# Kernel tuning notes

Hardware: AMD Instinct MI355X
Metric: run time of the kernel (lower is better)

Reference implementation:

```python
import jax, jax.numpy as jnp
import numpy as np

# ---- static config (from init_kwargs) ----
N = 500_000            # total points
B = 4                  # batch size (lidar frames)
VX, VY, VZ = 0.2, 0.2, 4.0
PC = (0.0, -40.0, -3.0, 70.4, 40.0, 1.0)  # point cloud range
NZ = int((PC[5] - PC[2]) / VZ)   # 1
NY = int((PC[4] - PC[1]) / VY)   # 400
NX = int((PC[3] - PC[0]) / VX)   # 352
CANVAS = B * NZ * NY * NX        # dense voxel canvas (563200)
EPS = 1e-3                       # BN eps
XOFF = VX / 2 + PC[0]
YOFF = VY / 2 + PC[1]
ZOFF = VZ / 2 + PC[2]
C0, C1 = 64, 128                 # feat_channels
CIN = 13                         # 4 + 2(spatial) + 3(cluster) + 3(center) + 1(dist)


def setup_inputs() -> dict:
    key = jax.random.key(0)
    ks = jax.random.split(key, 12)
    # points uniformly in the point-cloud range, plus intensity
    xyz = jax.random.uniform(ks[0], (N, 3), dtype=jnp.float32) \
        * jnp.array([70.4, 80.0, 4.0], jnp.float32) \
        + jnp.array([0.0, -40.0, -3.0], jnp.float32)
    inten = jax.random.uniform(ks[1], (N, 1), dtype=jnp.float32)
    features = jnp.concatenate([xyz, inten], axis=1)  # (N, 4)
    # voxel coords consistent with the points; batch idx sorted so coors[-1,0]==B-1
    bidx = jnp.sort(jax.random.randint(ks[2], (N,), 0, B, dtype=jnp.int32))
    zc = jnp.clip(((xyz[:, 2] - PC[2]) / VZ).astype(jnp.int32), 0, NZ - 1)
    yc = jnp.clip(((xyz[:, 1] - PC[1]) / VY).astype(jnp.int32), 0, NY - 1)
    xc = jnp.clip(((xyz[:, 0] - PC[0]) / VX).astype(jnp.int32), 0, NX - 1)
    coors = jnp.stack([bidx, zc, yc, xc], axis=1)  # (N, 4) [b, z, y, x]
    # VFE weights (Linear bias=False) + BN affine params
    s0 = 1.0 / np.sqrt(CIN)
    s1 = 1.0 / np.sqrt(2 * C0)
    s2 = 1.0 / np.sqrt(C1 + 2)
    W0 = jax.random.uniform(ks[3], (CIN, C0), jnp.float32, -s0, s0)
    g0 = jnp.ones((C0,), jnp.float32)
    b0 = jnp.zeros((C0,), jnp.float32)
    W1 = jax.random.uniform(ks[4], (2 * C0, C1), jnp.float32, -s1, s1)
    g1 = jnp.ones((C1,), jnp.float32)
    b1 = jnp.zeros((C1,), jnp.float32)
    Ws = jax.random.uniform(ks[5], (C1 + 2, C1), jnp.float32, -s2, s2)
    bs = jax.random.uniform(ks[6], (C1,), jnp.float32, -s2, s2)
    return {"features": features, "coors": coors,
            "W0": W0, "g0": g0, "b0": b0,
            "W1": W1, "g1": g1, "b1": b1,
            "Ws": Ws, "bs": bs}


def _bn_relu(x, g, b):
    # BN1d in training mode: batch statistics (biased var), eps=1e-3
    m = jnp.mean(x, axis=0)
    v = jnp.var(x, axis=0)
    return jax.nn.relu((x - m) * jax.lax.rsqrt(v + EPS) * g + b)


def reference(features, coors, W0, g0, b0, W1, g1, b1, Ws, bs):
    xyz = features[:, :3]
    # linear voxel id on the dense canvas: b*Z*Y*X + z*Y*X + y*X + x
    v = ((coors[:, 0] * NZ + coors[:, 1]) * NY + coors[:, 2]) * NX + coors[:, 3]
    v = v.astype(jnp.int32)

    # ---- calculate_spatial_features (unique + index_add -> segment reductions) ----
    counts = jax.ops.segment_sum(jnp.ones((N,), features.dtype), v, CANVAS)
    safe = jnp.maximum(counts, 1.0)                       # clamp(min=1)
    density = safe / (VX * VY * VZ)                       # per-voxel point density
    sum_coords = jax.ops.segment_sum(xyz, v, CANVAS)      # (CANVAS, 3)
    voxel_mean = sum_coords / safe[:, None]
    point_mean = voxel_mean[v]                            # gather back to points
    pdist = jnp.linalg.norm(xyz - point_mean, axis=1)
    mean_dist = (jax.ops.segment_sum(pdist, v, CANVAS) / safe)[v]
    f_spatial = jnp.stack([density[v], mean_dist], axis=1)  # (N, 2)

    # ---- cluster center (avg scatter + gather): same voxel mean ----
    f_cluster = xyz - point_mean                          # (N, 3)

    # ---- voxel center offsets ----
    cf = coors.astype(features.dtype)
    f_center = jnp.stack([
        xyz[:, 0] - (cf[:, 3] * VX + XOFF),
        xyz[:, 1] - (cf[:, 2] * VY + YOFF),
        xyz[:, 2] - (cf[:, 1] * VZ + ZOFF)], axis=1)      # (N, 3)

    # ---- distance ----
    f_dist = jnp.linalg.norm(xyz, axis=1, keepdims=True)  # (N, 1)

    x = jnp.concatenate([features, f_spatial, f_cluster, f_center, f_dist], axis=1)  # (N, 13)

    # ---- VFE layer 0: Linear -> BN -> ReLU, scatter-max, gather, concat ----
    p = _bn_relu(x @ W0, g0, b0)                          # (N, 64)
    vmax = jax.ops.segment_max(p, v, CANVAS)              # (CANVAS, 64), -inf on empty
    x = jnp.concatenate([p, vmax[v]], axis=1)             # (N, 128)

    # ---- VFE layer 1 + feature_scaling ----
    p = _bn_relu(x @ W1, g1, b1)                          # (N, 128)
    p = jax.nn.relu(jnp.concatenate([p, f_spatial], axis=1) @ Ws + bs)  # (N, 128)
    return p  # return_point_feats=True
```

## Files before the change

### kernel.cpp

```cpp
#include <hip/hip_runtime.h>
#include <hip/hip_bf16.h>

#define NZv 1
#define NYv 400
#define NXv 352
#define Bv 4
#define CANVASv (Bv * NZv * NYv * NXv)
#define EPSF 0.001f
#define VXF 0.2f
#define VYF 0.2f
#define VZF 4.0f
#define XOFFv 0.1f
#define YOFFv -39.9f
#define ZOFFv -1.0f

typedef __attribute__((ext_vector_type(8))) short bf16x8;
typedef __attribute__((ext_vector_type(4))) float f32x4;
typedef __attribute__((ext_vector_type(2))) unsigned int u32x2;

__device__ __forceinline__ short f2bf(float f) {
    union { __hip_bfloat16 h; short s; } u;
    u.h = __float2bfloat16(f);
    return u.s;
}
__device__ __forceinline__ float bf2f(short s) {
    return __uint_as_float(((unsigned int)(unsigned short)s) << 16);
}
__device__ __forceinline__ unsigned int pk(float a, float b) {
    return (unsigned int)(unsigned short)f2bf(a) | ((unsigned int)(unsigned short)f2bf(b) << 16);
}

struct MomTab { signed char a[105]; signed char b[105]; };
constexpr MomTab make_momtab() {
    MomTab m{};
    int idx = 0;
    for (int a = 0; a < 14; ++a)
        for (int b = a; b < 14; ++b) { m.a[idx] = (signed char)a; m.b[idx] = (signed char)b; ++idx; }
    return m;
}
constexpr MomTab MT = make_momtab();

__global__ void k_scatter1(const int4* __restrict__ coors, int* __restrict__ vidx,
                           float* __restrict__ counts, int n)
{
    int i = blockIdx.x * blockDim.x + threadIdx.x;
    if (i >= n) return;
    int4 c = coors[i];
    int v = ((c.x * NZv + c.y) * NYv + c.z) * NXv + c.w;
    vidx[i] = v;
    atomicAdd(&counts[v], 1.0f);
}

__global__ __launch_bounds__(1024) void k_scanA(const float* __restrict__ counts,
                                                int* __restrict__ starts, int* __restrict__ bsum)
{
    __shared__ int sdata[1024];
    int t = threadIdx.x;
    int v = blockIdx.x * 1024 + t;
    int c = (int)counts[v];
    sdata[t] = c;
    __syncthreads();
#pragma unroll
    for (int off = 1; off < 1024; off <<= 1) {
        int val = (t >= off) ? sdata[t - off] : 0;
        __syncthreads();
        sdata[t] += val;
        __syncthreads();
    }
    starts[v] = sdata[t] - c;
    if (t == 1023) bsum[blockIdx.x] = sdata[t];
}

__global__ __launch_bounds__(1024) void k_scanBC(const int* __restrict__ bsum,
                                                 int* __restrict__ starts)
{
    __shared__ int red[16];
    int b = blockIdx.x, t = threadIdx.x;
    int v = (t < b) ? bsum[t] : 0;
    for (int m = 1; m < 64; m <<= 1) v += __shfl_xor(v, m);
    int lane = t & 63, w = t >> 6;
    if (lane == 0) red[w] = v;
    __syncthreads();
    if (t == 0) {
        int s = 0;
#pragma unroll
        for (int q = 0; q < 16; ++q) s += red[q];
        red[0] = s;
    }
    __syncthreads();
    starts[b * 1024 + t] += red[0];
}

__global__ void k_perm(const int* __restrict__ vidx, int* __restrict__ starts,
                       int* __restrict__ perm, int n)
{
    int i = blockIdx.x * blockDim.x + threadIdx.x;
    if (i >= n) return;
    int pos = atomicAdd(&starts[vidx[i]], 1);
    perm[pos] = i;
}

__global__ __launch_bounds__(256) void k_seg(const float4* __restrict__ feat,
                                             const int* __restrict__ startsPost,
                                             const int* __restrict__ perm,
                                             float4* __restrict__ vstat, int nvox)
{
    int stride = gridDim.x * blockDim.x;
    for (int v = blockIdx.x * blockDim.x + threadIdx.x; v < nvox; v += stride) {
        int end = startsPost[v];
        int begin = (v > 0) ? startsPost[v - 1] : 0;
        if (begin == end) continue;
        float sx = 0.f, sy = 0.f, sz = 0.f;
        for (int j = begin; j < end; ++j) {
            float4 f = feat[perm[j]];
            sx += f.x; sy += f.y; sz += f.z;
        }
        float inv = 1.0f / (float)(end - begin);
        float mx = sx * inv, my = sy * inv, mz = sz * inv;
        float pd = 0.f;
        for (int j = begin; j < end; ++j) {
            float4 f = feat[perm[j]];
            float dx = f.x - mx, dy = f.y - my, dz = f.z - mz;
            pd += sqrtf(dx * dx + dy * dy + dz * dz);
        }
        vstat[v] = make_float4(mx, my, mz, pd * inv);
    }
}

__global__ __launch_bounds__(256, 1) void k_prexm(const float4* __restrict__ feat,
                       const int4* __restrict__ coors,
                       const int* __restrict__ vidx, const float* __restrict__ counts,
                       const float4* __restrict__ vstat,
                       unsigned int* __restrict__ x, unsigned int* __restrict__ fspc,
                       double* __restrict__ md0, int n)
{
    float acc[105];
#pragma unroll
    for (int e = 0; e < 105; ++e) acc[e] = 0.f;
    int t = threadIdx.x;
    int stride = gridDim.x * blockDim.x;
    for (int i = blockIdx.x * blockDim.x + t; i < n; i += stride) {
        float4 f = feat[i];
        int4 c = coors[i];
        int v = vidx[i];
        float safe = fmaxf(counts[v], 1.0f);
        float4 vs = vstat[v];
        float vals[14];
        vals[0] = f.x; vals[1] = f.y; vals[2] = f.z; vals[3] = f.w;
        vals[4] = safe / 0.16f;
        vals[5] = vs.w;
        vals[6] = f.x - vs.x;
        vals[7] = f.y - vs.y;
        vals[8] = f.z - vs.z;
        vals[9]  = f.x - ((float)c.w * VXF + XOFFv);
        vals[10] = f.y - ((float)c.z * VYF + YOFFv);
        vals[11] = f.z - ((float)c.y * VZF + ZOFFv);
        vals[12] = sqrtf(f.x * f.x + f.y * f.y + f.z * f.z);
        vals[13] = 1.0f;
        unsigned int row[8];
#pragma unroll
        for (int q = 0; q < 6; ++q) row[q] = pk(vals[2 * q], vals[2 * q + 1]);
        row[6] = pk(vals[12], 0.f);
        row[7] = 0u;
        uint4* dst = (uint4*)(x + (size_t)i * 8);
        dst[0] = make_uint4(row[0], row[1], row[2], row[3]);
        dst[1] = make_uint4(row[4], row[5], row[6], row[7]);
        fspc[i] = row[2];
        float qv[14];
#pragma unroll
        for (int k = 0; k < 13; ++k)
            qv[k] = bf2f((short)((k & 1) ? (row[k >> 1] >> 16) : (row[k >> 1] & 0xFFFF)));
        qv[13] = 1.0f;
#pragma unroll
        for (int e = 0; e < 105; ++e)
            acc[e] = fmaf(qv[MT.a[e]], qv[MT.b[e]], acc[e]);
    }
    __shared__ float wacc[4][105];
    int lane = t & 63, wid = t >> 6;
#pragma unroll
    for (int e = 0; e < 105; ++e) {
        float v = acc[e];
        v += __shfl_xor(v, 1);
        v += __shfl_xor(v, 2);
        v += __shfl_xor(v, 4);
        v += __shfl_xor(v, 8);
        v += __shfl_xor(v, 16);
        v += __shfl_xor(v, 32);
        if (lane == 0) wacc[wid][e] = v;
    }
    __syncthreads();
    if (t < 105) {
        double s = (double)wacc[0][t] + (double)wacc[1][t] + (double)wacc[2][t] + (double)wacc[3][t];
        atomicAdd(&md0[t], s);
    }
}

__device__ __forceinline__ int idx14(int a, int b) {
    return a * 14 - a * (a - 1) / 2 + (b - a);
}

__global__ void k_fin0(const double* __restrict__ md0, const float* __restrict__ W0,
                       const float* __restrict__ g0, const float* __restrict__ b0,
                       float* __restrict__ sc0, float* __restrict__ sh0, int n)
{
    __shared__ double mom[105];
    int t = threadIdx.x;
    for (int e = t; e < 105; e += 64) mom[e] = md0[e];
    __syncthreads();
    double nn = (double)n;
    double mu[13];
#pragma unroll
    for (int j = 0; j < 13; ++j) mu[j] = mom[idx14(j, 13)] / nn;
    double wc[13];
#pragma unroll
    for (int j = 0; j < 13; ++j) wc[j] = (double)W0[j * 64 + t];
    double meanc = 0.0, var = 0.0;
#pragma unroll
    for (int j = 0; j < 13; ++j) {
        meanc += mu[j] * wc[j];
        for (int k = 0; k < 13; ++k) {
            int a = j < k ? j : k, b = j < k ? k : j;
            double cov = mom[idx14(a, b)] / nn - mu[j] * mu[k];
            var += cov * wc[j] * wc[k];
        }
    }
    float scale = g0[t] * rsqrtf((float)var + EPSF);
    sc0[t] = scale;
    sh0[t] = b0[t] - (float)meanc * scale;
}

__global__ __launch_bounds__(256) void k_vmaxv(const unsigned int* __restrict__ x,
    const float* __restrict__ W0, const float* __restrict__ sc0, const float* __restrict__ sh0,
    const int* __restrict__ startsPost, const int* __restrict__ perm,
    unsigned int* __restrict__ p0, unsigned int* __restrict__ vmaxb, int nvox)
{
    int t = threadIdx.x, lane = t & 63, wid = t >> 6;
    float wcol[13];
#pragma unroll
    for (int k = 0; k < 13; ++k) wcol[k] = W0[k * 64 + lane];
    float sc = sc0[lane], sh = sh0[lane];
    int nw = gridDim.x * 4;
    for (int v = blockIdx.x * 4 + wid; v < nvox; v += nw) {
        int end = startsPost[v];
        int begin = (v > 0) ? startsPost[v - 1] : 0;
        if (begin == end) continue;
        float m = 0.f;
        for (int j = begin; j < end; ++j) {
            int i = perm[j];
            const uint4* xr = (const uint4*)(x + (size_t)i * 8);
            uint4 r0 = xr[0], r1 = xr[1];
            unsigned int rw[8] = {r0.x, r0.y, r0.z, r0.w, r1.x, r1.y, r1.z, r1.w};
            float acc = 0.f;
#pragma unroll
            for (int k = 0; k < 13; ++k) {
                float xv = bf2f((short)((k & 1) ? (rw[k >> 1] >> 16) : (rw[k >> 1] & 0xFFFF)));
                acc = fmaf(xv, wcol[k], acc);
            }
            float pv = fmaxf(fmaf(acc, sc, sh), 0.f);
            float pn = __shfl_xor(pv, 1);
            if ((lane & 1) == 0)
                p0[(size_t)i * 32 + (lane >> 1)] = pk(pv, pn);
            m = fmaxf(m, pv);
        }
        float mn = __shfl_xor(m, 1);
        if ((lane & 1) == 0)
            vmaxb[(size_t)v * 32 + (lane >> 1)] = pk(m, mn);
    }
}

#define G1_SW1 0
#define G1_SX  32768
#define G1_ST  65536
#define G1_LDS (65536 + 8192)

__global__ __launch_bounds__(512) void k_gemm1s(const unsigned int* __restrict__ p0,
    const unsigned int* __restrict__ vmaxb, const int* __restrict__ vidx,
    const float* __restrict__ W1, unsigned int* __restrict__ y1,
    double* __restrict__ s1d, double* __restrict__ sq1d, int n, int ntiles)
{
    extern __shared__ char lds[];
    char* sW1 = lds + G1_SW1;
    char* sx  = lds + G1_SX;
    int t = threadIdx.x, lane = t & 63, w = t >> 6;
    int pl = lane & 15, qd = lane >> 4;

#pragma unroll
    for (int it = 0; it < 8; ++it) {
        int e = (it * 512 + t) * 4;
        float4 wv = *(const float4*)(W1 + e);
        int k = e >> 7, c0 = e & 127;
        float wa[4] = {wv.x, wv.y, wv.z, wv.w};
#pragma unroll
        for (int qq = 0; qq < 4; ++qq) {
            int c = c0 + qq;
            *(short*)(sW1 + c * 256 + ((k * 2) ^ ((c & 7) << 4))) = f2bf(wa[qq]);
        }
    }
    __syncthreads();

    float st_s[8][4], st_q[8][4];
#pragma unroll
    for (int cb = 0; cb < 8; ++cb)
#pragma unroll
        for (int jj = 0; jj < 4; ++jj) { st_s[cb][jj] = 0.f; st_q[cb][jj] = 0.f; }

    unsigned int szr = (unsigned int)(pl & 7) << 4;
    int rb_ = w * 16 + pl;
    for (int tile = blockIdx.x; tile < ntiles; tile += gridDim.x) {
        int base = tile * 128;
        {
            int p = t >> 2, s = t & 3;
            int i = base + p;
            char* rowp = sx + p * 256;
            unsigned int sz = (unsigned int)(p & 7) << 4;
            uint4 d0, d1, d2, d3;
            if (i < n) {
                const uint4* src = (s < 2)
                    ? (const uint4*)(p0 + (size_t)i * 32 + s * 16)
                    : (const uint4*)(vmaxb + (size_t)vidx[i] * 32 + (s - 2) * 16);
                d0 = src[0]; d1 = src[1]; d2 = src[2]; d3 = src[3];
            } else {
                d0 = d1 = d2 = d3 = make_uint4(0u, 0u, 0u, 0u);
            }
            int k2 = s * 64;
            *(uint4*)(rowp + ((k2 +  0) ^ sz)) = d0;
            *(uint4*)(rowp + ((k2 + 16) ^ sz)) = d1;
            *(uint4*)(rowp + ((k2 + 32) ^ sz)) = d2;
            *(uint4*)(rowp + ((k2 + 48) ^ sz)) = d3;
        }
        __syncthreads();
        f32x4 acc[8];
#pragma unroll
        for (int cb = 0; cb < 8; ++cb) acc[cb] = (f32x4){0.f, 0.f, 0.f, 0.f};
#pragma unroll
        for (int kc = 0; kc < 4; ++kc) {
            int ko2 = kc * 64 + qd * 16;
            bf16x8 b = *(bf16x8*)(sx + rb_ * 256 + (ko2 ^ szr));
#pragma unroll
            for (int cb = 0; cb < 8; ++cb) {
                int ra_ = cb * 16 + pl;
                bf16x8 a = *(bf16x8*)(sW1 + ra_ * 256 + (ko2 ^ szr));
                acc[cb] = __builtin_amdgcn_mfma_f32_16x16x32_bf16(a, b, acc[cb], 0, 0, 0);
            }
        }
        int pt = base + rb_;
        if (pt < n) {
            char* yrow = (char*)y1 + (size_t)pt * 256 + qd * 8;
#pragma unroll
            for (int cb = 0; cb < 8; ++cb) {
                u32x2 o;
                o.x = pk(acc[cb][0], acc[cb][1]);
                o.y = pk(acc[cb][2], acc[cb][3]);
                *(u32x2*)(yrow + cb * 32) = o;
#pragma unroll
                for (int jj = 0; jj < 4; ++jj) {
                    float av = acc[cb][jj];
                    st_s[cb][jj] += av;
                    st_q[cb][jj] = fmaf(av, av, st_q[cb][jj]);
                }
            }
        }
        __syncthreads();
    }
    float* ssum = (float*)(lds + G1_ST);
    float* ssq  = ssum + 8 * 128;
#pragma unroll
    for (int cb = 0; cb < 8; ++cb)
#pragma unroll
        for (int jj = 0; jj < 4; ++jj) {
            float sv = st_s[cb][jj], qv = st_q[cb][jj];
            sv += __shfl_xor(sv, 1); qv += __shfl_xor(qv, 1);
            sv += __shfl_xor(sv, 2); qv += __shfl_xor(qv, 2);
            sv += __shfl_xor(sv, 4); qv += __shfl_xor(qv, 4);
            sv += __shfl_xor(sv, 8); qv += __shfl_xor(qv, 8);
            if (pl == 0) {
                int ch = cb * 16 + qd * 4 + jj;
                ssum[w * 128 + ch] = sv;
                ssq[w * 128 + ch] = qv;
            }
        }
    __syncthreads();
    if (t < 128) {
        float s = 0.f, q = 0.f;
#pragma unroll
        for (int ww = 0; ww < 8; ++ww) { s += ssum[ww * 128 + t]; q += ssq[ww * 128 + t]; }
        atomicAdd(&s1d[t], (double)s);
        atomicAdd(&sq1d[t], (double)q);
    }
}

__global__ void k_fin1s(const double* __restrict__ s1d, const double* __restrict__ sq1d,
                        const float* __restrict__ g1, const float* __restrict__ b1,
                        float* __restrict__ sc1, float* __restrict__ sh1, int n)
{
    int c = threadIdx.x;
    double mean = s1d[c] / (double)n;
    double var = sq1d[c] / (double)n - mean * mean;
    float scale = g1[c] * rsqrtf((float)var + EPSF);
    sc1[c] = scale;
    sh1[c] = b1[c] - (float)mean * scale;
}

#define F2_SWS 0
#define F2_SX  49152
#define F2_SCL (49152 + 24576)
#define F2_LDS (F2_SCL + 1536)

__global__ __launch_bounds__(256) void k_fused2(const uint4* __restrict__ y1,
    const unsigned int* __restrict__ fspc,
    const float* __restrict__ Wsp, const float* __restrict__ bsp,
    const float* __restrict__ sc1, const float* __restrict__ sh1,
    float* __restrict__ out, int n, int ntiles)
{
    extern __shared__ char lds[];
    char* sWs = lds + F2_SWS;
    char* sx  = lds + F2_SX;
    float* ssc = (float*)(lds + F2_SCL);
    float* ssh = ssc + 128;
    float* sbs = ssh + 128;
    int t = threadIdx.x, lane = t & 63, w = t >> 6;
    int pl = lane & 15, qd = lane >> 4;

    for (int it = 0; it < 17; ++it) {
        int e = (it * 256 + t) * 4;
        if (e < 16640) {
            float4 wv = *(const float4*)(Wsp + e);
            int k = e >> 7, c0 = e & 127;
            float wa[4] = {wv.x, wv.y, wv.z, wv.w};
#pragma unroll
            for (int qq = 0; qq < 4; ++qq) {
                int c = c0 + qq;
                *(short*)(sWs + c * 384 + ((k * 2) ^ ((c & 7) << 4))) = f2bf(wa[qq]);
            }
        }
    }
    for (int e = t; e < 128 * 15; e += 256) {
        int r = e / 15, qq = e - r * 15;
        int k2 = 260 + 4 * qq;
        *(unsigned int*)(sWs + r * 384 + (k2 ^ ((r & 7) << 4))) = 0u;
    }
    for (int e = t; e < 64 * 15; e += 256) {
        int r = e / 15, qq = e - r * 15;
        int k2 = 260 + 4 * qq;
        *(unsigned int*)(sx + r * 384 + (k2 ^ ((r & 7) << 4))) = 0u;
    }
    if (t < 128) { ssc[t] = sc1[t]; ssh[t] = sh1[t]; sbs[t] = bsp[t]; }
    __syncthreads();

    unsigned int szr = (unsigned int)(pl & 7) << 4;
    int rb_ = w * 16 + pl;
    for (int tile = blockIdx.x; tile < ntiles; tile += gridDim.x) {
        int base = tile * 64;
        {
            int p = t >> 2, s = t & 3;
            int i = base + p;
            char* rowp = sx + p * 384;
            unsigned int sz = (unsigned int)(p & 7) << 4;
            unsigned int ow[16];
            if (i < n) {
                const uint4* src = (const uint4*)((const char*)y1 + (size_t)i * 256 + s * 64);
                uint4 d0 = src[0], d1 = src[1], d2 = src[2], d3 = src[3];
                unsigned int iw[16] = {d0.x, d0.y, d0.z, d0.w, d1.x, d1.y, d1.z, d1.w,
                                       d2.x, d2.y, d2.z, d2.w, d3.x, d3.y, d3.z, d3.w};
#pragma unroll
                for (int qq = 0; qq < 16; ++qq) {
                    int c = s * 32 + 2 * qq;
                    float a = fmaxf(fmaf(bf2f((short)(iw[qq] & 0xFFFF)), ssc[c], ssh[c]), 0.f);
                    float b = fmaxf(fmaf(bf2f((short)(iw[qq] >> 16)), ssc[c + 1], ssh[c + 1]), 0.f);
                    ow[qq] = pk(a, b);
                }
            } else {
#pragma unroll
                for (int qq = 0; qq < 16; ++qq) ow[qq] = 0u;
            }
            int k2 = s * 64;
#pragma unroll
            for (int qq = 0; qq < 4; ++qq)
                *(uint4*)(rowp + ((k2 + 16 * qq) ^ sz)) =
                    make_uint4(ow[4 * qq], ow[4 * qq + 1], ow[4 * qq + 2], ow[4 * qq + 3]);
        }
        if (t < 64) {
            int i = base + t; if (i >= n) i = n - 1;
            unsigned int fs = fspc[i];
            *(unsigned int*)(sx + t * 384 + (256 ^ ((t & 7) << 4))) = fs;
        }
        __syncthreads();
        f32x4 acc[8];
#pragma unroll
        for (int cb = 0; cb < 8; ++cb) acc[cb] = (f32x4){0.f, 0.f, 0.f, 0.f};
#pragma unroll
        for (int kc = 0; kc < 5; ++kc) {
            int ko2 = kc * 64 + qd * 16;
            bf16x8 b = *(bf16x8*)(sx + rb_ * 384 + (ko2 ^ szr));
#pragma unroll
            for (int cb = 0; cb < 8; ++cb) {
                int ra_ = cb * 16 + pl;
                bf16x8 a = *(bf16x8*)(sWs + ra_ * 384 + (ko2 ^ szr));
                acc[cb] = __builtin_amdgcn_mfma_f32_16x16x32_bf16(a, b, acc[cb], 0, 0, 0);
            }
        }
        int pt = base + rb_;
        if (pt < n) {
            float* orow = out + (size_t)pt * 128 + qd * 4;
#pragma unroll
            for (int cb = 0; cb < 8; ++cb) {
                float4 bb = *(float4*)(sbs + cb * 16 + qd * 4);
                f32x4 o;
                o[0] = fmaxf(acc[cb][0] + bb.x, 0.f);
                o[1] = fmaxf(acc[cb][1] + bb.y, 0.f);
                o[2] = fmaxf(acc[cb][2] + bb.z, 0.f);
                o[3] = fmaxf(acc[cb][3] + bb.w, 0.f);
                __builtin_nontemporal_store(o, (f32x4*)(orow + cb * 16));
            }
        }
        __syncthreads();
    }
}

extern "C" void kernel_launch(void* const* d_in, const int* in_sizes, int n_in,
                              void* d_out, int out_size, void* d_ws, size_t ws_size,
                              hipStream_t stream)
{
    const float* feat = (const float*)d_in[0];
    const int*   coor = (const int*)d_in[1];
    const float* W0   = (const float*)d_in[2];
    const float* g0   = (const float*)d_in[3];
    const float* b0   = (const float*)d_in[4];
    const float* W1   = (const float*)d_in[5];
    const float* g1   = (const float*)d_in[6];
    const float* b1   = (const float*)d_in[7];
    const float* Wsp  = (const float*)d_in[8];
    const float* bsp  = (const float*)d_in[9];
    float* outp = (float*)d_out;

    int n = in_sizes[0] / 4;
    size_t npad = ((size_t)n + 127) & ~127ULL;

    char* ws = (char*)d_ws;
    size_t off = 0;
    auto alloc = [&](size_t bytes) { char* p = ws + off; off = (off + bytes + 255) & ~255ULL; return p; };
    int*          vidx   = (int*)alloc(npad * 4);
    float*        counts = (float*)alloc((size_t)CANVASv * 4);
    double*       md0    = (double*)alloc(105 * 8 + 256 * 8);
    double*       s1d    = (double*)((char*)md0 + 105 * 8);
    double*       sq1d   = s1d + 128;
    float4*       vstat  = (float4*)alloc((size_t)CANVASv * 16);
    unsigned int* x      = (unsigned int*)alloc(npad * 32);
    unsigned int* fspc   = (unsigned int*)alloc(npad * 4);
    unsigned int* p0     = (unsigned int*)alloc(npad * 128);
    unsigned int* vmaxb  = (unsigned int*)alloc((size_t)CANVASv * 128);
    unsigned int* y1     = (unsigned int*)alloc(npad * 256);
    int*          starts = (int*)alloc((size_t)CANVASv * 4);
    int*          perm   = (int*)alloc(npad * 4);
    int*          bsum   = (int*)alloc(1024 * 4);
    float*        sc0    = (float*)alloc(64 * 4);
    float*        sh0    = (float*)alloc(64 * 4);
    float*        sc1    = (float*)alloc(128 * 4);
    float*        sh1    = (float*)alloc(128 * 4);
    if (off > ws_size) return;

    hipMemsetAsync(counts, 0, (size_t)CANVASv * 4 + 105 * 8 + 256 * 8, stream);

    int blocksN = (n + 255) / 256;
    k_scatter1<<<blocksN, 256, 0, stream>>>((const int4*)coor, vidx, counts, n);

    k_scanA<<<CANVASv / 1024, 1024, 0, stream>>>(counts, starts, bsum);
    k_scanBC<<<CANVASv / 1024, 1024, 0, stream>>>(bsum, starts);
    k_perm<<<blocksN, 256, 0, stream>>>(vidx, starts, perm, n);

    k_seg<<<1024, 256, 0, stream>>>((const float4*)feat, starts, perm, vstat, CANVASv);

    k_prexm<<<512, 256, 0, stream>>>((const float4*)feat, (const int4*)coor, vidx, counts, vstat, x, fspc, md0, n);
    k_fin0<<<1, 64, 0, stream>>>(md0, W0, g0, b0, sc0, sh0, n);

    k_vmaxv<<<2048, 256, 0, stream>>>(x, W0, sc0, sh0, starts, perm, p0, vmaxb, CANVASv);

    int ntiles1 = (n + 127) / 128;
    hipFuncSetAttribute((const void*)k_gemm1s, hipFuncAttributeMaxDynamicSharedMemorySize, G1_LDS);
    k_gemm1s<<<512, 512, G1_LDS, stream>>>(p0, vmaxb, vidx, W1, y1, s1d, sq1d, n, ntiles1);

    k_fin1s<<<1, 128, 0, stream>>>(s1d, sq1d, g1, b1, sc1, sh1, n);

    int ntiles2 = (n + 63) / 64;
    hipFuncSetAttribute((const void*)k_fused2, hipFuncAttributeMaxDynamicSharedMemorySize, F2_LDS);
    k_fused2<<<512, 256, F2_LDS, stream>>>((const uint4*)y1, fspc, Wsp, bsp, sc1, sh1, outp, n, ntiles2);
}
```

Before: 434.2 us.

## Recompute layer-1 GEMM in final kernel instead of materializing y1

The layer-1 GEMM kernel now only accumulates BN statistics and no longer writes the bf16 y1 intermediate. The final fused kernel regathers p0 and vmax rows, recomputes the W1 GEMM, applies BN+ReLU in LDS, then runs the scaling GEMM. This trades a 128 MB-scale write and read of y1 for a second pass of GEMM1 compute and a repeated gather. The fused kernel uses more LDS (about 130 KB) and larger 512-thread blocks on a 256-block grid, which lowers occupancy.

After: 409.3 us, median of 2. -5.7%, faster.

```diff
diff --git a/kernel.cpp b/kernel.cpp
--- a/kernel.cpp
+++ b/kernel.cpp
@@ -273,9 +273,9 @@
 #define G1_ST  65536
 #define G1_LDS (65536 + 8192)
 
-__global__ __launch_bounds__(512) void k_gemm1s(const unsigned int* __restrict__ p0,
+__global__ __launch_bounds__(512) void k_gstat(const unsigned int* __restrict__ p0,
     const unsigned int* __restrict__ vmaxb, const int* __restrict__ vidx,
-    const float* __restrict__ W1, unsigned int* __restrict__ y1,
+    const float* __restrict__ W1,
     double* __restrict__ s1d, double* __restrict__ sq1d, int n, int ntiles)
 {
     extern __shared__ char lds[];
@@ -345,20 +345,14 @@
         }
         int pt = base + rb_;
         if (pt < n) {
-            char* yrow = (char*)y1 + (size_t)pt * 256 + qd * 8;
-#pragma unroll
-            for (int cb = 0; cb < 8; ++cb) {
-                u32x2 o;
-                o.x = pk(acc[cb][0], acc[cb][1]);
-                o.y = pk(acc[cb][2], acc[cb][3]);
-                *(u32x2*)(yrow + cb * 32) = o;
+#pragma unroll
+            for (int cb = 0; cb < 8; ++cb)
 #pragma unroll
                 for (int jj = 0; jj < 4; ++jj) {
                     float av = acc[cb][jj];
                     st_s[cb][jj] += av;
                     st_q[cb][jj] = fmaf(av, av, st_q[cb][jj]);
                 }
-            }
         }
         __syncthreads();
     }
@@ -401,28 +395,43 @@
     sh1[c] = b1[c] - (float)mean * scale;
 }
 
-#define F2_SWS 0
-#define F2_SX  49152
-#define F2_SCL (49152 + 24576)
-#define F2_LDS (F2_SCL + 1536)
-
-__global__ __launch_bounds__(256) void k_fused2(const uint4* __restrict__ y1,
+#define F3_SW1 0
+#define F3_SWS 32768
+#define F3_SX  (32768 + 49152)
+#define F3_SCL (32768 + 49152 + 49152)
+#define F3_LDS (F3_SCL + 1536)
+
+__global__ __launch_bounds__(512) void k_fused3(const unsigned int* __restrict__ p0,
+    const unsigned int* __restrict__ vmaxb, const int* __restrict__ vidx,
     const unsigned int* __restrict__ fspc,
-    const float* __restrict__ Wsp, const float* __restrict__ bsp,
+    const float* __restrict__ W1, const float* __restrict__ Wsp, const float* __restrict__ bsp,
     const float* __restrict__ sc1, const float* __restrict__ sh1,
     float* __restrict__ out, int n, int ntiles)
 {
     extern __shared__ char lds[];
-    char* sWs = lds + F2_SWS;
-    char* sx  = lds + F2_SX;
-    float* ssc = (float*)(lds + F2_SCL);
+    char* sW1 = lds + F3_SW1;
+    char* sWs = lds + F3_SWS;
+    char* sx  = lds + F3_SX;
+    float* ssc = (float*)(lds + F3_SCL);
     float* ssh = ssc + 128;
     float* sbs = ssh + 128;
     int t = threadIdx.x, lane = t & 63, w = t >> 6;
     int pl = lane & 15, qd = lane >> 4;
 
-    for (int it = 0; it < 17; ++it) {
-        int e = (it * 256 + t) * 4;
+#pragma unroll
+    for (int it = 0; it < 8; ++it) {
+        int e = (it * 512 + t) * 4;
+        float4 wv = *(const float4*)(W1 + e);
+        int k = e >> 7, c0 = e & 127;
+        float wa[4] = {wv.x, wv.y, wv.z, wv.w};
+#pragma unroll
+        for (int qq = 0; qq < 4; ++qq) {
+            int c = c0 + qq;
+            *(short*)(sW1 + c * 256 + ((k * 2) ^ ((c & 7) << 4))) = f2bf(wa[qq]);
+        }
+    }
+    for (int it = 0; it < 9; ++it) {
+        int e = (it * 512 + t) * 4;
         if (e < 16640) {
             float4 wv = *(const float4*)(Wsp + e);
             int k = e >> 7, c0 = e & 127;
@@ -434,15 +443,11 @@
             }
         }
     }
-    for (int e = t; e < 128 * 15; e += 256) {
+    for (int e = t; e < 128 * 15; e += 512) {
         int r = e / 15, qq = e - r * 15;
         int k2 = 260 + 4 * qq;
         *(unsigned int*)(sWs + r * 384 + (k2 ^ ((r & 7) << 4))) = 0u;
-    }
-    for (int e = t; e < 64 * 15; e += 256) {
-        int r = e / 15, qq = e - r * 15;
-        int k2 = 260 + 4 * qq;
-        *(unsigned int*)(sx + r * 384 + (k2 ^ ((r & 7) << 4))) = 0u;
+        *(unsigned int*)(sx  + r * 384 + (k2 ^ ((r & 7) << 4))) = 0u;
     }
     if (t < 128) { ssc[t] = sc1[t]; ssh[t] = sh1[t]; sbs[t] = bsp[t]; }
     __syncthreads();
@@ -450,44 +455,62 @@
     unsigned int szr = (unsigned int)(pl & 7) << 4;
     int rb_ = w * 16 + pl;
     for (int tile = blockIdx.x; tile < ntiles; tile += gridDim.x) {
-        int base = tile * 64;
+        int base = tile * 128;
         {
             int p = t >> 2, s = t & 3;
             int i = base + p;
             char* rowp = sx + p * 384;
             unsigned int sz = (unsigned int)(p & 7) << 4;
-            unsigned int ow[16];
+            uint4 d0, d1, d2, d3;
             if (i < n) {
-                const uint4* src = (const uint4*)((const char*)y1 + (size_t)i * 256 + s * 64);
-                uint4 d0 = src[0], d1 = src[1], d2 = src[2], d3 = src[3];
-                unsigned int iw[16] = {d0.x, d0.y, d0.z, d0.w, d1.x, d1.y, d1.z, d1.w,
-                                       d2.x, d2.y, d2.z, d2.w, d3.x, d3.y, d3.z, d3.w};
-#pragma unroll
-                for (int qq = 0; qq < 16; ++qq) {
-                    int c = s * 32 + 2 * qq;
-                    float a = fmaxf(fmaf(bf2f((short)(iw[qq] & 0xFFFF)), ssc[c], ssh[c]), 0.f);
-                    float b = fmaxf(fmaf(bf2f((short)(iw[qq] >> 16)), ssc[c + 1], ssh[c + 1]), 0.f);
-                    ow[qq] = pk(a, b);
-                }
+                const uint4* src = (s < 2)
+                    ? (const uint4*)(p0 + (size_t)i * 32 + s * 16)
+                    : (const uint4*)(vmaxb + (size_t)vidx[i] * 32 + (s - 2) * 16);
+                d0 = src[0]; d1 = src[1]; d2 = src[2]; d3 = src[3];
             } else {
-#pragma unroll
-                for (int qq = 0; qq < 16; ++qq) ow[qq] = 0u;
+                d0 = d1 = d2 = d3 = make_uint4(0u, 0u, 0u, 0u);
             }
             int k2 = s * 64;
-#pragma unroll
-            for (int qq = 0; qq < 4; ++qq)
-                *(uint4*)(rowp + ((k2 + 16 * qq) ^ sz)) =
-                    make_uint4(ow[4 * qq], ow[4 * qq + 1], ow[4 * qq + 2], ow[4 * qq + 3]);
-        }
-        if (t < 64) {
-            int i = base + t; if (i >= n) i = n - 1;
+            *(uint4*)(rowp + ((k2 +  0) ^ sz)) = d0;
+            *(uint4*)(rowp + ((k2 + 16) ^ sz)) = d1;
+            *(uint4*)(rowp + ((k2 + 32) ^ sz)) = d2;
+            *(uint4*)(rowp + ((k2 + 48) ^ sz)) = d3;
+        }
+        __syncthreads();
+        f32x4 acc1[8];
+#pragma unroll
+        for (int cb = 0; cb < 8; ++cb) acc1[cb] = (f32x4){0.f, 0.f, 0.f, 0.f};
+#pragma unroll
+        for (int kc = 0; kc < 4; ++kc) {
+            int ko2 = kc * 64 + qd * 16;
+            bf16x8 b = *(bf16x8*)(sx + rb_ * 384 + (ko2 ^ szr));
+#pragma unroll
+            for (int cb = 0; cb < 8; ++cb) {
+                int ra_ = cb * 16 + pl;
+                bf16x8 a = *(bf16x8*)(sW1 + ra_ * 256 + (ko2 ^ szr));
+                acc1[cb] = __builtin_amdgcn_mfma_f32_16x16x32_bf16(a, b, acc1[cb], 0, 0, 0);
+            }
+        }
+#pragma unroll
+        for (int cb = 0; cb < 8; ++cb) {
+            int ch0 = cb * 16 + qd * 4;
+            float v0 = fmaxf(fmaf(acc1[cb][0], ssc[ch0 + 0], ssh[ch0 + 0]), 0.f);
+            float v1 = fmaxf(fmaf(acc1[cb][1], ssc[ch0 + 1], ssh[ch0 + 1]), 0.f);
+            float v2 = fmaxf(fmaf(acc1[cb][2], ssc[ch0 + 2], ssh[ch0 + 2]), 0.f);
+            float v3 = fmaxf(fmaf(acc1[cb][3], ssc[ch0 + 3], ssh[ch0 + 3]), 0.f);
+            u32x2 o;
+            o.x = pk(v0, v1);
+            o.y = pk(v2, v3);
+            *(u32x2*)(sx + rb_ * 384 + ((unsigned int)(cb * 32 + qd * 8) ^ szr)) = o;
+        }
+        if (qd == 0) {
+            int i = base + rb_; if (i >= n) i = n - 1;
             unsigned int fs = fspc[i];
-            *(unsigned int*)(sx + t * 384 + (256 ^ ((t & 7) << 4))) = fs;
-        }
-        __syncthreads();
-        f32x4 acc[8];
-#pragma unroll
-        for (int cb = 0; cb < 8; ++cb) acc[cb] = (f32x4){0.f, 0.f, 0.f, 0.f};
+            *(unsigned int*)(sx + rb_ * 384 + (256u ^ szr)) = fs;
+        }
+        f32x4 acc2[8];
+#pragma unroll
+        for (int cb = 0; cb < 8; ++cb) acc2[cb] = (f32x4){0.f, 0.f, 0.f, 0.f};
 #pragma unroll
         for (int kc = 0; kc < 5; ++kc) {
             int ko2 = kc * 64 + qd * 16;
@@ -496,7 +519,7 @@
             for (int cb = 0; cb < 8; ++cb) {
                 int ra_ = cb * 16 + pl;
                 bf16x8 a = *(bf16x8*)(sWs + ra_ * 384 + (ko2 ^ szr));
-                acc[cb] = __builtin_amdgcn_mfma_f32_16x16x32_bf16(a, b, acc[cb], 0, 0, 0);
+                acc2[cb] = __builtin_amdgcn_mfma_f32_16x16x32_bf16(a, b, acc2[cb], 0, 0, 0);
             }
         }
         int pt = base + rb_;
@@ -506,10 +529,10 @@
             for (int cb = 0; cb < 8; ++cb) {
                 float4 bb = *(float4*)(sbs + cb * 16 + qd * 4);
                 f32x4 o;
-                o[0] = fmaxf(acc[cb][0] + bb.x, 0.f);
-                o[1] = fmaxf(acc[cb][1] + bb.y, 0.f);
-                o[2] = fmaxf(acc[cb][2] + bb.z, 0.f);
-                o[3] = fmaxf(acc[cb][3] + bb.w, 0.f);
+                o[0] = fmaxf(acc2[cb][0] + bb.x, 0.f);
+                o[1] = fmaxf(acc2[cb][1] + bb.y, 0.f);
+                o[2] = fmaxf(acc2[cb][2] + bb.z, 0.f);
+                o[3] = fmaxf(acc2[cb][3] + bb.w, 0.f);
                 __builtin_nontemporal_store(o, (f32x4*)(orow + cb * 16));
             }
         }
@@ -549,7 +572,6 @@
     unsigned int* fspc   = (unsigned int*)alloc(npad * 4);
     unsigned int* p0     = (unsigned int*)alloc(npad * 128);
     unsigned int* vmaxb  = (unsigned int*)alloc((size_t)CANVASv * 128);
-    unsigned int* y1     = (unsigned int*)alloc(npad * 256);
     int*          starts = (int*)alloc((size_t)CANVASv * 4);
     int*          perm   = (int*)alloc(npad * 4);
     int*          bsum   = (int*)alloc(1024 * 4);
@@ -575,13 +597,11 @@
 
     k_vmaxv<<<2048, 256, 0, stream>>>(x, W0, sc0, sh0, starts, perm, p0, vmaxb, CANVASv);
 
-    int ntiles1 = (n + 127) / 128;
-    hipFuncSetAttribute((const void*)k_gemm1s, hipFuncAttributeMaxDynamicSharedMemorySize, G1_LDS);
-    k_gemm1s<<<512, 512, G1_LDS, stream>>>(p0, vmaxb, vidx, W1, y1, s1d, sq1d, n, ntiles1);
-
+    int ntiles = (n + 127) / 128;
+    hipFuncSetAttribute((const void*)k_gstat, hipFuncAttributeMaxDynamicSharedMemorySize, G1_LDS);
+    k_gstat<<<512, 512, G1_LDS, stream>>>(p0, vmaxb, vidx, W1, s1d, sq1d, n, ntiles);
     k_fin1s<<<1, 128, 0, stream>>>(s1d, sq1d, g1, b1, sc1, sh1, n);
 
-    int ntiles2 = (n + 63) / 64;
-    hipFuncSetAttribute((const void*)k_fused2, hipFuncAttributeMaxDynamicSharedMemorySize, F2_LDS);
-    k_fused2<<<512, 256, F2_LDS, stream>>>((const uint4*)y1, fspc, Wsp, bsp, sc1, sh1, outp, n, ntiles2);
-}
+    hipFuncSetAttribute((const void*)k_fused3, hipFuncAttributeMaxDynamicSharedMemorySize, F3_LDS);
+    k_fused3<<<256, 512, F3_LDS, stream>>>(p0, vmaxb, vidx, fspc, W1, Wsp, bsp, sc1, sh1, outp, n, ntiles);
+}
```
